# Kernel optimization log

Hardware: AMD Instinct MI355X
Metric: run time of the kernel (lower is better)

The kernel has to match this reference:

```python
import jax, jax.numpy as jnp
import numpy as np

MIN_DEPTH = 0.1
MAX_DEPTH = 100.0
EPS = 1e-10


def setup_inputs() -> dict:
    key = jax.random.key(0)
    k1, k2, k3 = jax.random.split(key, 3)
    B, R, S = 4, 16384, 128
    colors = jax.random.uniform(k1, (B, R, S, 3), dtype=jnp.float32)
    density_logits = jax.random.normal(k2, (B, R, S, 1), dtype=jnp.float32)
    # depths must be monotonically increasing along the sample axis
    depths = jnp.sort(jax.random.uniform(k3, (B, R, S, 1), dtype=jnp.float32) * 50.0, axis=2)
    return {"colors": colors, "density_logits": density_logits, "depths": depths}


def reference(colors, density_logits, depths):
    # midpoints along the sample axis (dim 2)
    colors_mid = (colors[:, :, :-1] + colors[:, :, 1:]) * 0.5          # [B,R,S-1,3]
    dl_mid = (density_logits[:, :, :-1] + density_logits[:, :, 1:]) * 0.5
    depths_mid = (depths[:, :, :-1] + depths[:, :, 1:]) * 0.5          # [B,R,S-1,1]
    deltas = depths[:, :, 1:] - depths[:, :, :-1]

    # density_activation == 'softplus'
    densities_mid = jax.nn.softplus(dl_mid - 1.0)

    alpha = 1.0 - jnp.exp(-densities_mid * deltas)                     # [B,R,S-1,1]
    alpha_shifted = jnp.concatenate(
        [jnp.ones_like(alpha[:, :, :1]), 1.0 - alpha + EPS], axis=-2)
    transmittance = jnp.cumprod(alpha_shifted, axis=-2)[:, :, :-1]
    weights = (alpha + EPS) * transmittance                            # [B,R,S-1,1]
    weight_total = weights.sum(axis=2)                                 # [B,R,1]

    # c_sky is None branch
    weights_all = weights
    composite_rgb = jnp.sum(weights * colors_mid, axis=-2)             # [B,R,3]
    composite_depth = jnp.sum(weights * depths_mid, axis=-2) / (EPS + weight_total)

    composite_depth = jnp.nan_to_num(composite_depth, nan=MAX_DEPTH)
    composite_depth = jnp.clip(composite_depth, MIN_DEPTH, MAX_DEPTH)
    composite_rgb = composite_rgb * 2.0 - 1.0
    return (composite_rgb, composite_depth, weights, weights_all, alpha, depths_mid)
```

## Files before the change

### kernel.cpp

```cpp
#include <hip/hip_runtime.h>
#include <math.h>

namespace {
constexpr int Bn = 4, Rn = 16384, Sn = 128;
constexpr int NRAY = Bn * Rn;
constexpr int SI   = Sn - 1;
constexpr size_t OFF_RGB   = 0;
constexpr size_t OFF_DEPTH = OFF_RGB   + (size_t)NRAY * 3;
constexpr size_t OFF_W     = OFF_DEPTH + (size_t)NRAY;
constexpr size_t OFF_WALL  = OFF_W     + (size_t)NRAY * SI;
constexpr size_t OFF_ALPHA = OFF_WALL  + (size_t)NRAY * SI;
constexpr size_t OFF_DMID  = OFF_ALPHA + (size_t)NRAY * SI;
constexpr float  EPSF  = 1e-10f;
constexpr float  LOG2E = 1.44269504088896340736f;
}

template <int ctrl, int rmask>
__device__ __forceinline__ float dpp_mov(float x, float oldv) {
    return __int_as_float(__builtin_amdgcn_update_dpp(
        __float_as_int(oldv), __float_as_int(x), ctrl, rmask, 0xf, false));
}

__device__ __forceinline__ float scan_mul(float x) {
    x *= dpp_mov<0x111, 0xf>(x, 1.0f);
    x *= dpp_mov<0x112, 0xf>(x, 1.0f);
    x *= dpp_mov<0x114, 0xf>(x, 1.0f);
    x *= dpp_mov<0x118, 0xf>(x, 1.0f);
    x *= dpp_mov<0x142, 0xa>(x, 1.0f);
    x *= dpp_mov<0x143, 0xc>(x, 1.0f);
    return x;
}

__device__ __forceinline__ float scan_add(float x) {
    x += dpp_mov<0x111, 0xf>(x, 0.0f);
    x += dpp_mov<0x112, 0xf>(x, 0.0f);
    x += dpp_mov<0x114, 0xf>(x, 0.0f);
    x += dpp_mov<0x118, 0xf>(x, 0.0f);
    x += dpp_mov<0x142, 0xa>(x, 0.0f);
    x += dpp_mov<0x143, 0xc>(x, 0.0f);
    return x;
}

__device__ __forceinline__ float next_lane(float x) {
    return dpp_mov<0x130, 0xf>(x, 0.0f);
}

__global__ __launch_bounds__(256) void raymarch_kernel(
    const float* __restrict__ colors,
    const float* __restrict__ dlog,
    const float* __restrict__ depths,
    float* __restrict__ out)
{
    const int gtid = blockIdx.x * 256 + threadIdx.x;
    const int ray  = gtid >> 6;
    const int lane = threadIdx.x & 63;

    const float2* dp = reinterpret_cast<const float2*>(depths) + (size_t)ray * (Sn / 2);
    const float2* gp = reinterpret_cast<const float2*>(dlog)   + (size_t)ray * (Sn / 2);
    const float2* cp = reinterpret_cast<const float2*>(colors) + (size_t)ray * (Sn * 3 / 2);

    float2 d  = dp[lane];
    float2 g  = gp[lane];
    float2 c0 = cp[lane * 3 + 0];
    float2 c1 = cp[lane * 3 + 1];
    float2 c2 = cp[lane * 3 + 2];

    float d2  = next_lane(d.x);
    float g2  = next_lane(g.x);
    float cnx = next_lane(c0.x);
    float cny = next_lane(c0.y);
    float cnz = next_lane(c1.x);

    const bool valid1 = (lane < 63);

    float delta0 = d.y - d.x;
    float dm0    = 0.5f * (d.x + d.y);
    float x0     = 0.5f * (g.x + g.y) - 1.0f;
    float cm0x   = 0.5f * (c0.x + c1.y);
    float cm0y   = 0.5f * (c0.y + c2.x);
    float cm0z   = 0.5f * (c1.x + c2.y);

    float delta1 = valid1 ? (d2 - d.y)                 : 0.0f;
    float dm1    = valid1 ? 0.5f * (d.y + d2)          : 0.0f;
    float x1     = valid1 ? (0.5f * (g.y + g2) - 1.0f) : 0.0f;
    float cm1x   = valid1 ? 0.5f * (c1.y + cnx)        : 0.0f;
    float cm1y   = valid1 ? 0.5f * (c2.x + cny)        : 0.0f;
    float cm1z   = valid1 ? 0.5f * (c2.y + cnz)        : 0.0f;

    float l0 = __log2f(1.0f + exp2f(x0 * LOG2E));
    float l1 = __log2f(1.0f + exp2f(x1 * LOG2E));
    float alpha0 = 1.0f - exp2f(-l0 * delta0);
    float alpha1 = 1.0f - exp2f(-l1 * delta1);
    float t0 = 1.0f - alpha0 + EPSF;
    float t1 = valid1 ? (1.0f - alpha1 + EPSF) : 1.0f;

    float s  = scan_mul(t0 * t1);
    float T0 = dpp_mov<0x138, 0xf>(s, 1.0f);
    float T1 = T0 * t0;

    float w0 = (alpha0 + EPSF) * T0;
    float w1 = valid1 ? (alpha1 + EPSF) * T1 : 0.0f;

    size_t base = (size_t)ray * SI + 2 * lane;
    out[OFF_W     + base] = w0;
    out[OFF_WALL  + base] = w0;
    out[OFF_ALPHA + base] = alpha0;
    out[OFF_DMID  + base] = dm0;
    if (valid1) {
        out[OFF_W     + base + 1] = w1;
        out[OFF_WALL  + base + 1] = w1;
        out[OFF_ALPHA + base + 1] = alpha1;
        out[OFF_DMID  + base + 1] = dm1;
    }

    float wsum = scan_add(w0 + w1);
    float rx   = scan_add(w0 * cm0x + w1 * cm1x);
    float ry   = scan_add(w0 * cm0y + w1 * cm1y);
    float rz   = scan_add(w0 * cm0z + w1 * cm1z);
    float dsum = scan_add(w0 * dm0 + w1 * dm1);

    if (lane == 63) {
        float cd = dsum / (EPSF + wsum);
        if (isnan(cd)) cd = 100.0f;
        cd = fminf(fmaxf(cd, 0.1f), 100.0f);
        out[OFF_RGB + (size_t)ray * 3 + 0] = rx * 2.0f - 1.0f;
        out[OFF_RGB + (size_t)ray * 3 + 1] = ry * 2.0f - 1.0f;
        out[OFF_RGB + (size_t)ray * 3 + 2] = rz * 2.0f - 1.0f;
        out[OFF_DEPTH + ray] = cd;
    }
}

extern "C" void kernel_launch(void* const* d_in, const int* in_sizes, int n_in,
                              void* d_out, int out_size, void* d_ws, size_t ws_size,
                              hipStream_t stream) {
    const float* colors = (const float*)d_in[0];
    const float* dlog   = (const float*)d_in[1];
    const float* depths = (const float*)d_in[2];
    float* out = (float*)d_out;

    dim3 grid(NRAY / 4);
    dim3 block(256);
    hipLaunchKernelGGL(raymarch_kernel, grid, block, 0, stream, colors, dlog, depths, out);
}
```

Baseline: 261.9 us.

## Persistent grid with prefetch and LDS-staged vectorized nontemporal output stores

The kernel becomes persistent with a fixed grid, and each block prefetches the next group of four rays while computing the current one. Per-sample outputs (weights, alpha, depth midpoints) are staged in shared memory so the block can write its 4x127 contiguous floats as 16-byte nontemporal vector stores, rather than as strided scalar stores from each lane. This targets store coalescing and load latency in a memory-bound kernel. In exchange it adds two block barriers per iteration and extra register pressure from the prefetched values.

```diff
diff --git a/kernel.cpp b/kernel.cpp
--- a/kernel.cpp
+++ b/kernel.cpp
@@ -5,6 +5,8 @@
 constexpr int Bn = 4, Rn = 16384, Sn = 128;
 constexpr int NRAY = Bn * Rn;
 constexpr int SI   = Sn - 1;
+constexpr int NG   = NRAY / 4;
+constexpr int GRID = 2048;
 constexpr size_t OFF_RGB   = 0;
 constexpr size_t OFF_DEPTH = OFF_RGB   + (size_t)NRAY * 3;
 constexpr size_t OFF_W     = OFF_DEPTH + (size_t)NRAY;
@@ -13,6 +15,7 @@
 constexpr size_t OFF_DMID  = OFF_ALPHA + (size_t)NRAY * SI;
 constexpr float  EPSF  = 1e-10f;
 constexpr float  LOG2E = 1.44269504088896340736f;
+typedef float f4 __attribute__((ext_vector_type(4)));
 }
 
 template <int ctrl, int rmask>
@@ -45,88 +48,131 @@
     return dpp_mov<0x130, 0xf>(x, 0.0f);
 }
 
-__global__ __launch_bounds__(256) void raymarch_kernel(
+__device__ __forceinline__ void load_ray(
+    const float* __restrict__ colors, const float* __restrict__ dlog,
+    const float* __restrict__ depths, int ray, int lane,
+    float2& d, float2& g, float2& c0, float2& c1, float2& c2)
+{
+    const float2* dp = reinterpret_cast<const float2*>(depths) + (size_t)ray * (Sn / 2);
+    const float2* gp = reinterpret_cast<const float2*>(dlog)   + (size_t)ray * (Sn / 2);
+    const float2* cp = reinterpret_cast<const float2*>(colors) + (size_t)ray * (Sn * 3 / 2);
+    d  = dp[lane];
+    g  = gp[lane];
+    c0 = cp[lane * 3 + 0];
+    c1 = cp[lane * 3 + 1];
+    c2 = cp[lane * 3 + 2];
+}
+
+__global__ __launch_bounds__(256, 8) void raymarch_kernel(
     const float* __restrict__ colors,
     const float* __restrict__ dlog,
     const float* __restrict__ depths,
     float* __restrict__ out)
 {
-    const int gtid = blockIdx.x * 256 + threadIdx.x;
-    const int ray  = gtid >> 6;
-    const int lane = threadIdx.x & 63;
+    __shared__ __attribute__((aligned(16))) float st[3 * 508];
 
-    const float2* dp = reinterpret_cast<const float2*>(depths) + (size_t)ray * (Sn / 2);
-    const float2* gp = reinterpret_cast<const float2*>(dlog)   + (size_t)ray * (Sn / 2);
-    const float2* cp = reinterpret_cast<const float2*>(colors) + (size_t)ray * (Sn * 3 / 2);
+    const int tid  = threadIdx.x;
+    const int wv   = tid >> 6;
+    const int lane = tid & 63;
 
-    float2 d  = dp[lane];
-    float2 g  = gp[lane];
-    float2 c0 = cp[lane * 3 + 0];
-    float2 c1 = cp[lane * 3 + 1];
-    float2 c2 = cp[lane * 3 + 2];
+    int g = blockIdx.x;
+    float2 d, dg, c0, c1, c2;
+    load_ray(colors, dlog, depths, 4 * g + wv, lane, d, dg, c0, c1, c2);
 
-    float d2  = next_lane(d.x);
-    float g2  = next_lane(g.x);
-    float cnx = next_lane(c0.x);
-    float cny = next_lane(c0.y);
-    float cnz = next_lane(c1.x);
+    while (true) {
+        const int gn = g + GRID;
+        const bool has_next = (gn < NG);
+        float2 d_n, dg_n, c0_n, c1_n, c2_n;
+        if (has_next)
+            load_ray(colors, dlog, depths, 4 * gn + wv, lane, d_n, dg_n, c0_n, c1_n, c2_n);
 
-    const bool valid1 = (lane < 63);
+        float d2  = next_lane(d.x);
+        float g2  = next_lane(dg.x);
+        float cnx = next_lane(c0.x);
+        float cny = next_lane(c0.y);
+        float cnz = next_lane(c1.x);
 
-    float delta0 = d.y - d.x;
-    float dm0    = 0.5f * (d.x + d.y);
-    float x0     = 0.5f * (g.x + g.y) - 1.0f;
-    float cm0x   = 0.5f * (c0.x + c1.y);
-    float cm0y   = 0.5f * (c0.y + c2.x);
-    float cm0z   = 0.5f * (c1.x + c2.y);
+        const bool valid1 = (lane < 63);
 
-    float delta1 = valid1 ? (d2 - d.y)                 : 0.0f;
-    float dm1    = valid1 ? 0.5f * (d.y + d2)          : 0.0f;
-    float x1     = valid1 ? (0.5f * (g.y + g2) - 1.0f) : 0.0f;
-    float cm1x   = valid1 ? 0.5f * (c1.y + cnx)        : 0.0f;
-    float cm1y   = valid1 ? 0.5f * (c2.x + cny)        : 0.0f;
-    float cm1z   = valid1 ? 0.5f * (c2.y + cnz)        : 0.0f;
+        float delta0 = d.y - d.x;
+        float dm0    = 0.5f * (d.x + d.y);
+        float x0     = 0.5f * (dg.x + dg.y) - 1.0f;
+        float cm0x   = 0.5f * (c0.x + c1.y);
+        float cm0y   = 0.5f * (c0.y + c2.x);
+        float cm0z   = 0.5f * (c1.x + c2.y);
 
-    float l0 = __log2f(1.0f + exp2f(x0 * LOG2E));
-    float l1 = __log2f(1.0f + exp2f(x1 * LOG2E));
-    float alpha0 = 1.0f - exp2f(-l0 * delta0);
-    float alpha1 = 1.0f - exp2f(-l1 * delta1);
-    float t0 = 1.0f - alpha0 + EPSF;
-    float t1 = valid1 ? (1.0f - alpha1 + EPSF) : 1.0f;
+        float delta1 = valid1 ? (d2 - d.y)                   : 0.0f;
+        float dm1    = valid1 ? 0.5f * (d.y + d2)            : 0.0f;
+        float x1     = valid1 ? (0.5f * (dg.y + g2) - 1.0f)  : 0.0f;
+        float cm1x   = valid1 ? 0.5f * (c1.y + cnx)          : 0.0f;
+        float cm1y   = valid1 ? 0.5f * (c2.x + cny)          : 0.0f;
+        float cm1z   = valid1 ? 0.5f * (c2.y + cnz)          : 0.0f;
 
-    float s  = scan_mul(t0 * t1);
-    float T0 = dpp_mov<0x138, 0xf>(s, 1.0f);
-    float T1 = T0 * t0;
+        float l0 = __log2f(1.0f + exp2f(x0 * LOG2E));
+        float l1 = __log2f(1.0f + exp2f(x1 * LOG2E));
+        float alpha0 = 1.0f - exp2f(-l0 * delta0);
+        float alpha1 = 1.0f - exp2f(-l1 * delta1);
+        float t0 = 1.0f - alpha0 + EPSF;
+        float t1 = valid1 ? (1.0f - alpha1 + EPSF) : 1.0f;
 
-    float w0 = (alpha0 + EPSF) * T0;
-    float w1 = valid1 ? (alpha1 + EPSF) * T1 : 0.0f;
+        float s  = scan_mul(t0 * t1);
+        float T0 = dpp_mov<0x138, 0xf>(s, 1.0f);
+        float T1 = T0 * t0;
 
-    size_t base = (size_t)ray * SI + 2 * lane;
-    out[OFF_W     + base] = w0;
-    out[OFF_WALL  + base] = w0;
-    out[OFF_ALPHA + base] = alpha0;
-    out[OFF_DMID  + base] = dm0;
-    if (valid1) {
-        out[OFF_W     + base + 1] = w1;
-        out[OFF_WALL  + base + 1] = w1;
-        out[OFF_ALPHA + base + 1] = alpha1;
-        out[OFF_DMID  + base + 1] = dm1;
-    }
+        float w0 = (alpha0 + EPSF) * T0;
+        float w1 = valid1 ? (alpha1 + EPSF) * T1 : 0.0f;
 
-    float wsum = scan_add(w0 + w1);
-    float rx   = scan_add(w0 * cm0x + w1 * cm1x);
-    float ry   = scan_add(w0 * cm0y + w1 * cm1y);
-    float rz   = scan_add(w0 * cm0z + w1 * cm1z);
-    float dsum = scan_add(w0 * dm0 + w1 * dm1);
+        const int c = wv * SI + 2 * lane;
+        st[c]            = w0;
+        st[508 + c]      = alpha0;
+        st[1016 + c]     = dm0;
+        if (valid1) {
+            st[c + 1]        = w1;
+            st[508 + c + 1]  = alpha1;
+            st[1016 + c + 1] = dm1;
+        }
 
-    if (lane == 63) {
-        float cd = dsum / (EPSF + wsum);
-        if (isnan(cd)) cd = 100.0f;
-        cd = fminf(fmaxf(cd, 0.1f), 100.0f);
-        out[OFF_RGB + (size_t)ray * 3 + 0] = rx * 2.0f - 1.0f;
-        out[OFF_RGB + (size_t)ray * 3 + 1] = ry * 2.0f - 1.0f;
-        out[OFF_RGB + (size_t)ray * 3 + 2] = rz * 2.0f - 1.0f;
-        out[OFF_DEPTH + ray] = cd;
+        float wsum = scan_add(w0 + w1);
+        float rx   = scan_add(w0 * cm0x + w1 * cm1x);
+        float ry   = scan_add(w0 * cm0y + w1 * cm1y);
+        float rz   = scan_add(w0 * cm0z + w1 * cm1z);
+        float dsum = scan_add(w0 * dm0 + w1 * dm1);
+
+        if (lane == 63) {
+            const int ray = 4 * g + wv;
+            float cd = dsum / (EPSF + wsum);
+            if (isnan(cd)) cd = 100.0f;
+            cd = fminf(fmaxf(cd, 0.1f), 100.0f);
+            out[OFF_RGB + (size_t)ray * 3 + 0] = rx * 2.0f - 1.0f;
+            out[OFF_RGB + (size_t)ray * 3 + 1] = ry * 2.0f - 1.0f;
+            out[OFF_RGB + (size_t)ray * 3 + 2] = rz * 2.0f - 1.0f;
+            out[OFF_DEPTH + ray] = cd;
+        }
+
+        __syncthreads();
+
+        {
+            constexpr size_t arrOFF[4] = { OFF_W, OFF_WALL, OFF_ALPHA, OFF_DMID };
+            const size_t blockbase = (size_t)508 * g;
+            #pragma unroll
+            for (int pass = 0; pass < 2; ++pass) {
+                const int q = tid + 256 * pass;
+                const int a = q >> 7;
+                const int j = q & 127;
+                if (j < 127) {
+                    const int srcreg = (a < 2) ? 0 : (a - 1);
+                    f4 v = *reinterpret_cast<const f4*>(st + srcreg * 508 + 4 * j);
+                    __builtin_nontemporal_store(
+                        v, reinterpret_cast<f4*>(out + arrOFF[a] + blockbase + 4 * j));
+                }
+            }
+        }
+
+        __syncthreads();
+
+        if (!has_next) break;
+        g = gn;
+        d = d_n; dg = dg_n; c0 = c0_n; c1 = c1_n; c2 = c2_n;
     }
 }
 
@@ -138,7 +184,6 @@
     const float* depths = (const float*)d_in[2];
     float* out = (float*)d_out;
 
-    dim3 grid(NRAY / 4);
-    dim3 block(256);
-    hipLaunchKernelGGL(raymarch_kernel, grid, block, 0, stream, colors, dlog, depths, out);
+    hipLaunchKernelGGL(raymarch_kernel, dim3(GRID), dim3(256), 0, stream,
+                       colors, dlog, depths, out);
 }
```

Result: slower. 268.5 us (+2.5%).
